# Optimization experiments

Measured on AMD Instinct MI355X. Metric: run time of the kernel, lower is better.

The kernel has to match this reference:

```python
import jax, jax.numpy as jnp
import numpy as np

K_KNN = 20
TC = 3  # taylor_channel
N_TERMS = 20  # trivariate polynomial terms up to order 3
CHANNELS = [(6, 32), (32, 64), (64, 128), (128, 256)]


def _knn_indices(xyz, k):
    sq = jnp.sum(xyz * xyz, axis=1)  # B x N
    d2 = sq[:, :, None] + sq[:, None, :] - 2.0 * jnp.einsum('bci,bcj->bij', xyz, xyz)
    _, idx = jax.lax.top_k(-d2, k)
    return idx


def _group(feat, idx):
    # feat: B x C x N, idx: B x N x K -> B x C x N x K
    return jax.vmap(lambda f, i: f[:, i])(feat, idx)


def _taylor_terms(g):
    X, Y, Z = g[:, 0], g[:, 1], g[:, 2]
    one = jnp.ones_like(X)
    terms = [one, X, Y, Z, X * Y, X * Z, Y * Z, X * X, Y * Y, Z * Z,
             X * X * Y, X * X * Z, X * Y * Y, Y * Y * Z, X * Z * Z, Y * Z * Z,
             X * Y * Z, X * X * X, Y * Y * Y, Z * Z * Z]
    return jnp.stack(terms, axis=1)


def _spider_conv(feat, idx, terms, w1, b1, w2, b2):
    # feat: B x C x N; w1: tc x 20; w2: out x (C*tc) x K
    B, C, N = feat.shape
    g = _group(feat, idx)  # B x C x N x K
    taylor = jnp.einsum('btnk,ot->bonk', terms, w1) + b1[None, :, None, None]
    g = (g[:, :, None, :, :] * taylor[:, None, :, :, :]).reshape(B, C * TC, N, g.shape[-1])
    out = jnp.einsum('bcnk,ock->bon', g, w2) + b2[None, :, None]
    return jax.nn.relu(out)


def _forward(pc, params):
    # pc: B x N x 6
    pcT = jnp.transpose(pc, (0, 2, 1))
    xyz = pcT[:, 0:3, :]
    idx = _knn_indices(xyz, K_KNN)  # B x N x K
    grouped_xyz = _group(xyz, idx)
    grouped_pc = grouped_xyz - xyz[:, :, :, None]  # relative coords
    terms = _taylor_terms(grouped_pc)
    feat = pcT
    feats = []
    for l in range(4):
        w1, b1, w2, b2 = params[l]
        feat = _spider_conv(feat, idx, terms, w1, b1, w2, b2)
        feats.append(feat)
    cat = jnp.concatenate(feats, axis=1)
    top2, _ = jax.lax.top_k(cat, 2)  # topk over point dim (last axis)
    return top2.reshape(cat.shape[0], -1)  # B x 960


def setup_inputs() -> dict:
    key = jax.random.key(0)
    keys = jax.random.split(key, 1 + 16)
    B, N = 4, 2048
    inp = {'pc': jax.random.normal(keys[0], (B, N, 6), dtype=jnp.float32)}
    ki = 1
    for l, (cin, cout) in enumerate(CHANNELS):
        inp[f'w1_{l}'] = jax.random.normal(keys[ki], (TC, N_TERMS), dtype=jnp.float32) * 0.1; ki += 1
        inp[f'b1_{l}'] = jax.random.normal(keys[ki], (TC,), dtype=jnp.float32) * 0.01; ki += 1
        inp[f'w2_{l}'] = jax.random.normal(keys[ki], (cout, cin * TC, K_KNN), dtype=jnp.float32) * (1.0 / np.sqrt(cin * TC * K_KNN)); ki += 1
        inp[f'b2_{l}'] = jax.random.normal(keys[ki], (cout,), dtype=jnp.float32) * 0.01; ki += 1
    return inp


def reference(pc, w1_0, b1_0, w2_0, b2_0, w1_1, b1_1, w2_1, b2_1,
              w1_2, b1_2, w2_2, b2_2, w1_3, b1_3, w2_3, b2_3):
    params = [(w1_0, b1_0, w2_0, b2_0), (w1_1, b1_1, w2_1, b2_1),
              (w1_2, b1_2, w2_2, b2_2), (w1_3, b1_3, w2_3, b2_3)]
    return _forward(pc, params)
```

## Files before the change

### kernel.cpp

```cpp
#include <hip/hip_runtime.h>
#include <math.h>

#define BB 4
#define NN 2048
#define KNN 20

typedef _Float16 f16x8 __attribute__((ext_vector_type(8)));
typedef _Float16 f16x4 __attribute__((ext_vector_type(4)));
typedef _Float16 f16x2 __attribute__((ext_vector_type(2)));
typedef float f32x4 __attribute__((ext_vector_type(4)));

#define DPP_STEP(CTRL, RMASK)                                                   \
    {                                                                           \
        unsigned ov = (unsigned)__builtin_amdgcn_update_dpp(                    \
            (int)bv, (int)bv, CTRL, RMASK, 0xf, false);                         \
        unsigned oj = (unsigned)__builtin_amdgcn_update_dpp(                    \
            (int)jj, (int)jj, CTRL, RMASK, 0xf, false);                         \
        bool lt = (ov < bv) || (ov == bv && oj < jj);                           \
        bv = lt ? ov : bv;                                                      \
        jj = lt ? oj : jj;                                                      \
    }

__global__ __launch_bounds__(256) void knn_kernel(const float* __restrict__ pc,
                                                  int* __restrict__ idx_out,
                                                  float* __restrict__ rel_out) {
    __shared__ float sx[NN], sy[NN], sz[NN], sq[NN];
    const int tid = threadIdx.x;
    const int b = blockIdx.x / (NN / 4);
    const int grp = blockIdx.x % (NN / 4);
    for (int p = tid; p < NN; p += 256) {
        float x = pc[(size_t)(b * NN + p) * 6 + 0];
        float y = pc[(size_t)(b * NN + p) * 6 + 1];
        float z = pc[(size_t)(b * NN + p) * 6 + 2];
        sx[p] = x; sy[p] = y; sz[p] = z;
        sq[p] = __fadd_rn(__fadd_rn(__fmul_rn(x, x), __fmul_rn(y, y)), __fmul_rn(z, z));
    }
    __syncthreads();
    const int lane = tid & 63;
    const int i = grp * 4 + (tid >> 6);
    const float xi = sx[i], yi = sy[i], zi = sz[i];
    const float sqi = sq[i];

    unsigned mmr[32];
#pragma unroll
    for (int t = 0; t < 32; ++t) {
        const int j = t * 64 + lane;
        float dot = __fadd_rn(__fadd_rn(__fmul_rn(xi, sx[j]), __fmul_rn(yi, sy[j])),
                              __fmul_rn(zi, sz[j]));
        float d2 = __fsub_rn(__fadd_rn(sqi, sq[j]), __fmul_rn(2.0f, dot));
        unsigned bbits = __float_as_uint(d2);
        mmr[t] = bbits ^ (0x80000000u | (unsigned)((int)bbits >> 31));
    }

    const unsigned UMAX = 0xFFFFFFFFu;
    unsigned mask = 0u;
    unsigned v1, t1, v2, t2;

    auto refill = [&]() {
        v1 = UMAX; t1 = 0u; v2 = UMAX; t2 = 0u;
#pragma unroll
        for (int t = 0; t < 32; ++t) {
            unsigned m = ((mask >> t) & 1u) ? UMAX : mmr[t];
            bool c1 = m < v1;
            bool c2 = m < v2;
            unsigned nv2 = c1 ? v1 : (c2 ? m : v2);
            unsigned nt2 = c1 ? t1 : (c2 ? (unsigned)t : t2);
            v1 = c1 ? m : v1;
            t1 = c1 ? (unsigned)t : t1;
            v2 = nv2; t2 = nt2;
        }
    };
    refill();

    const size_t orow = (size_t)(b * NN + i);
    for (int k = 0; k < KNN; ++k) {
        unsigned bv = v1;
        unsigned jj = (t1 << 6) | (unsigned)lane;
        DPP_STEP(0x111, 0xf)
        DPP_STEP(0x112, 0xf)
        DPP_STEP(0x114, 0xf)
        DPP_STEP(0x118, 0xf)
        DPP_STEP(0x142, 0xa)
        DPP_STEP(0x143, 0xc)
        const unsigned sj = (unsigned)__builtin_amdgcn_readlane((int)jj, 63);
        if (lane == 0) {
            idx_out[orow * KNN + k] = (int)sj;
            size_t ro = (orow * KNN + k) * 3;
            rel_out[ro + 0] = __fsub_rn(sx[sj], xi);
            rel_out[ro + 1] = __fsub_rn(sy[sj], yi);
            rel_out[ro + 2] = __fsub_rn(sz[sj], zi);
        }
        if (k < KNN - 1) {
            bool am = ((sj & 63u) == (unsigned)lane);
            if (am) {
                mask |= (1u << (sj >> 6));
                v1 = v2; t1 = t2; v2 = UMAX;
            }
            if (__ballot(v1 == UMAX) != 0ull) refill();
        }
    }
}

__global__ __launch_bounds__(256) void taylor_all_kernel(
    const float* __restrict__ rel,
    const float* __restrict__ w10, const float* __restrict__ b10, float* __restrict__ ty0,
    const float* __restrict__ w11, const float* __restrict__ b11, float* __restrict__ ty1,
    const float* __restrict__ w12, const float* __restrict__ b12, float* __restrict__ ty2,
    const float* __restrict__ w13, const float* __restrict__ b13, float* __restrict__ ty3) {
    __shared__ float w1s[4][60];
    __shared__ float b1s[4][3];
    const int tid = threadIdx.x;
    if (tid < 240) {
        const float* wp = (tid < 60) ? w10 : (tid < 120) ? w11 : (tid < 180) ? w12 : w13;
        w1s[tid / 60][tid % 60] = wp[tid % 60];
    } else if (tid < 252) {
        int r = tid - 240;
        const float* bp = (r < 3) ? b10 : (r < 6) ? b11 : (r < 9) ? b12 : b13;
        b1s[r / 3][r % 3] = bp[r % 3];
    }
    __syncthreads();
    int t = blockIdx.x * 256 + tid;
    if (t >= BB * NN * KNN) return;
    float X = rel[(size_t)t * 3 + 0], Y = rel[(size_t)t * 3 + 1], Z = rel[(size_t)t * 3 + 2];
    float tm[20];
    tm[0] = 1.f; tm[1] = X; tm[2] = Y; tm[3] = Z;
    tm[4] = X * Y; tm[5] = X * Z; tm[6] = Y * Z;
    tm[7] = X * X; tm[8] = Y * Y; tm[9] = Z * Z;
    tm[10] = X * X * Y; tm[11] = X * X * Z; tm[12] = X * Y * Y; tm[13] = Y * Y * Z;
    tm[14] = X * Z * Z; tm[15] = Y * Z * Z; tm[16] = X * Y * Z;
    tm[17] = X * X * X; tm[18] = Y * Y * Y; tm[19] = Z * Z * Z;
    float* typ[4] = {ty0, ty1, ty2, ty3};
#pragma unroll
    for (int l = 0; l < 4; ++l) {
#pragma unroll
        for (int o = 0; o < 3; ++o) {
            float a = b1s[l][o];
#pragma unroll
            for (int q = 0; q < 20; ++q) a += w1s[l][o * 20 + q] * tm[q];
            typ[l][(size_t)t * 3 + o] = a;
        }
    }
}

struct WsplitArgs {
    const float* w2[4];
    _Float16* wf[4];
    int COUT[4], CIN[4], CPAD[4], OCB[4], KCB[4];
    int cum[4];
};

__global__ __launch_bounds__(256) void wsplit_all_kernel(WsplitArgs a) {
    int e = blockIdx.x * 256 + threadIdx.x;
    if (e >= a.cum[3]) return;
    int l = (e >= a.cum[0]) + (e >= a.cum[1]) + (e >= a.cum[2]);
    int base = l ? a.cum[l - 1] : 0;
    e -= base;
    const int KCB = a.KCB[l], OCB = a.OCB[l], CPAD = a.CPAD[l], CIN = a.CIN[l];
    int i = e & 7;
    int lane = (e >> 3) & 63;
    int fi = e >> 9;
    int kcb = fi % KCB;
    int ocb = (fi / KCB) % OCB;
    int k = fi / (KCB * OCB);
    int oc = ocb * 16 + (lane & 15);
    int kk = kcb * 32 + (lane >> 4) * 8 + i;
    int o = kk / CPAD, c = kk % CPAD;
    float x = 0.f;
    if (o < 3 && c < CIN)
        x = a.w2[l][((size_t)oc * (CIN * 3) + c * 3 + o) * KNN + k];
    a.wf[l][e] = (_Float16)x;
}

template <int CIN, int COUT, int CK3P, int NT, int WM, int WN, int FM, int FN,
          int OCT, int KSPLIT, bool L0S>
__global__ __launch_bounds__(256) void convm_kernel(const float* __restrict__ fin,
                                                    const int* __restrict__ idx,
                                                    const float* __restrict__ tyg,
                                                    const _Float16* __restrict__ wf,
                                                    float* __restrict__ out) {
    constexpr int KR = KNN / KSPLIT;
    constexpr int SR = CK3P + 8;
    constexpr int KCB = CK3P / 32;
    constexpr int OCB = COUT / 16;
    constexpr int OCBLK = WM * FM * 16;
    constexpr int NTL = NN / NT;
    constexpr int TPR = 256 / NT;
    constexpr int CT = L0S ? 6 : (CIN / TPR);
    constexpr int CQ = L0S ? 2 : (CT / 4);
    static_assert(WN * FN * 16 == NT, "n tiling");
    static_assert(OCBLK * OCT == COUT, "oc tiling");
    static_assert(WM * WN == 4, "4 waves");
    static_assert(OCT * KSPLIT == 4 && NTL == 32 && NT == 64, "xcd decode");

    __shared__ _Float16 Bs[NT * SR];
    __shared__ _Float16 tyt[NT][3 * KR];
    __shared__ int idxt[NT][KR];

    const int tid = threadIdx.x;
    const int lane = tid & 63;
    const int wid = tid >> 6;
    const int wm = wid / WN;
    const int wn = wid % WN;
    const int bid = blockIdx.x;
    const int e_ = (bid & 7) >> 1;
    const int oct = e_ / KSPLIT;
    const int ks = e_ % KSPLIT;
    const int hi = ((bid >> 3) << 1) | (bid & 1);
    const int ntl = hi & 31;
    const int b = hi >> 5;
    const int n0 = ntl * NT;
    const int oc0 = oct * OCBLK;
    const int k0 = ks * KR;
    const size_t brow = (size_t)b * NN;

    for (int e = tid; e < NT * KR; e += 256) {
        int n = e / KR, kk = e % KR;
        idxt[n][kk] = idx[(brow + n0 + n) * KNN + k0 + kk];
    }
    for (int e = tid; e < NT * 3 * KR; e += 256) {
        int n = e / (3 * KR), q = e % (3 * KR);
        tyt[n][q] = (_Float16)tyg[((brow + n0 + n) * KNN + k0) * 3 + q];
    }
    __syncthreads();

    const int nrow = tid & 63;
    const int sub = tid >> 6;
    float4 g[CQ];

    auto issue_gather = [&](int kk) {
        if constexpr (L0S) {
            if (tid < 192) {
                int j = idxt[nrow][kk];
                const float* p = fin + (brow + j) * 6;
                g[0] = *reinterpret_cast<const float4*>(p);
                float2 r2 = *reinterpret_cast<const float2*>(p + 4);
                g[1].x = r2.x; g[1].y = r2.y;
            }
        } else {
            int j = idxt[nrow][kk];
            const float* p = fin + (brow + j) * CIN + sub * CT;
#pragma unroll
            for (int q = 0; q < CQ; ++q)
                g[q] = *reinterpret_cast<const float4*>(p + q * 4);
        }
    };
    issue_gather(0);

    f32x4 acc[FM][FN];
#pragma unroll
    for (int fm = 0; fm < FM; ++fm)
#pragma unroll
        for (int fn = 0; fn < FN; ++fn) acc[fm][fn] = (f32x4){0.f, 0.f, 0.f, 0.f};

    auto loadA = [&](int k, int kcb, f16x8* a) {
#pragma unroll
        for (int fm = 0; fm < FM; ++fm) {
            size_t fidx = ((size_t)k * OCB + (oc0 >> 4) + wm * FM + fm) * KCB + kcb;
            a[fm] = *reinterpret_cast<const f16x8*>(&wf[(fidx * 64 + lane) * 8]);
        }
    };
    auto loadB = [&](int kcb, f16x8* bb) {
#pragma unroll
        for (int fn = 0; fn < FN; ++fn) {
            int row = wn * FN * 16 + fn * 16 + (lane & 15);
            bb[fn] = *reinterpret_cast<const f16x8*>(
                &Bs[row * SR + kcb * 32 + (lane >> 4) * 8]);
        }
    };

    for (int kk = 0; kk < KR; ++kk) {
        const int k = k0 + kk;
        __syncthreads();
        if constexpr (L0S) {
            if (tid < 192) {
                _Float16 th = tyt[nrow][kk * 3 + sub];
                f16x2 tb; tb[0] = th; tb[1] = th;
                f16x2 g0, g1, g2;
                g0[0] = (_Float16)g[0].x; g0[1] = (_Float16)g[0].y;
                g1[0] = (_Float16)g[0].z; g1[1] = (_Float16)g[0].w;
                g2[0] = (_Float16)g[1].x; g2[1] = (_Float16)g[1].y;
                f16x2 p0 = g0 * tb, p1 = g1 * tb, p2 = g2 * tb;
                f16x8 hv;
                hv[0] = p0[0]; hv[1] = p0[1]; hv[2] = p1[0]; hv[3] = p1[1];
                hv[4] = p2[0]; hv[5] = p2[1]; hv[6] = (_Float16)0.f; hv[7] = (_Float16)0.f;
                *reinterpret_cast<f16x8*>(&Bs[nrow * SR + sub * 8]) = hv;
                if (sub == 0) {
                    f16x8 z = {};
                    *reinterpret_cast<f16x8*>(&Bs[nrow * SR + 24]) = z;
                }
            }
        } else {
            f16x2 gh[CT / 2];
#pragma unroll
            for (int q = 0; q < CQ; ++q) {
                f16x2 a0, a1;
                a0[0] = (_Float16)g[q].x; a0[1] = (_Float16)g[q].y;
                a1[0] = (_Float16)g[q].z; a1[1] = (_Float16)g[q].w;
                gh[2 * q] = a0; gh[2 * q + 1] = a1;
            }
            _Float16 th0 = tyt[nrow][kk * 3 + 0];
            _Float16 th1 = tyt[nrow][kk * 3 + 1];
            _Float16 th2 = tyt[nrow][kk * 3 + 2];
#pragma unroll
            for (int o = 0; o < 3; ++o) {
                _Float16 th = (o == 0) ? th0 : (o == 1) ? th1 : th2;
                f16x2 tb; tb[0] = th; tb[1] = th;
#pragma unroll
                for (int qp = 0; qp < CT / 8; ++qp) {
                    f16x2 p0 = gh[4 * qp + 0] * tb;
                    f16x2 p1 = gh[4 * qp + 1] * tb;
                    f16x2 p2 = gh[4 * qp + 2] * tb;
                    f16x2 p3 = gh[4 * qp + 3] * tb;
                    f16x8 hv;
                    hv[0] = p0[0]; hv[1] = p0[1]; hv[2] = p1[0]; hv[3] = p1[1];
                    hv[4] = p2[0]; hv[5] = p2[1]; hv[6] = p3[0]; hv[7] = p3[1];
                    *reinterpret_cast<f16x8*>(
                        &Bs[nrow * SR + o * CIN + sub * CT + qp * 8]) = hv;
                }
            }
        }
        __syncthreads();
        if (kk + 1 < KR) issue_gather(kk + 1);
        f16x8 aC[FM], bC[FN], aN[FM], bN[FN];
        loadA(k, 0, aC);
        loadB(0, bC);
#pragma unroll
        for (int kcb = 0; kcb < KCB; ++kcb) {
            if (kcb + 1 < KCB) { loadA(k, kcb + 1, aN); loadB(kcb + 1, bN); }
#pragma unroll
            for (int fm = 0; fm < FM; ++fm)
#pragma unroll
                for (int fn = 0; fn < FN; ++fn)
                    acc[fm][fn] = __builtin_amdgcn_mfma_f32_16x16x32_f16(
                        aC[fm], bC[fn], acc[fm][fn], 0, 0, 0);
            if (kcb + 1 < KCB) {
#pragma unroll
                for (int fm = 0; fm < FM; ++fm) aC[fm] = aN[fm];
#pragma unroll
                for (int fn = 0; fn < FN; ++fn) bC[fn] = bN[fn];
            }
        }
    }
    float* dst = out + (size_t)ks * ((size_t)BB * NN * COUT);
#pragma unroll
    for (int fm = 0; fm < FM; ++fm) {
        const int ocb = oc0 + wm * FM * 16 + fm * 16 + ((lane >> 4) << 2);
#pragma unroll
        for (int fn = 0; fn < FN; ++fn) {
            int n = n0 + wn * FN * 16 + fn * 16 + (lane & 15);
            float4 o4;
            o4.x = acc[fm][fn][0]; o4.y = acc[fm][fn][1];
            o4.z = acc[fm][fn][2]; o4.w = acc[fm][fn][3];
            *reinterpret_cast<float4*>(&dst[(brow + n) * COUT + ocb]) = o4;
        }
    }
}

template <int COUT, int KS>
__global__ __launch_bounds__(256) void combine_kernel(const float* __restrict__ p,
                                                      const float* __restrict__ b2,
                                                      float* __restrict__ out) {
    constexpr size_t TOT = (size_t)BB * NN * COUT;
    size_t i = (size_t)blockIdx.x * 256 + threadIdx.x;
    if (i * 4 >= TOT) return;
    const float4* p4 = reinterpret_cast<const float4*>(p);
    float4 a = p4[i];
#pragma unroll
    for (int s = 1; s < KS; ++s) {
        float4 v = p4[i + s * (TOT / 4)];
        a.x += v.x; a.y += v.y; a.z += v.z; a.w += v.w;
    }
    float4 bb = *reinterpret_cast<const float4*>(&b2[(i * 4) % COUT]);
    float4 r;
    r.x = fmaxf(a.x + bb.x, 0.f); r.y = fmaxf(a.y + bb.y, 0.f);
    r.z = fmaxf(a.z + bb.z, 0.f); r.w = fmaxf(a.w + bb.w, 0.f);
    reinterpret_cast<float4*>(out)[i] = r;
}

__global__ __launch_bounds__(256) void top2_kernel(const float* __restrict__ f1,
                                                   const float* __restrict__ f2,
                                                   const float* __restrict__ f3,
                                                   const float* __restrict__ p3,
                                                   const float* __restrict__ b23,
                                                   float* __restrict__ out) {
    __shared__ float m1s[256], m2s[256];
    const int bid = blockIdx.x;
    const int b = bid / 480;
    const int ch = bid % 480;
    const size_t brow = (size_t)b * NN;
    float m1 = -INFINITY, m2 = -INFINITY;
    if (ch < 224) {
        const float* f; int C, c;
        if (ch < 32)       { f = f1; C = 32;  c = ch; }
        else if (ch < 96)  { f = f2; C = 64;  c = ch - 32; }
        else               { f = f3; C = 128; c = ch - 96; }
        for (int n = threadIdx.x; n < NN; n += 256) {
            float v = f[(brow + n) * C + c];
            if (v > m1) { m2 = m1; m1 = v; }
            else if (v > m2) m2 = v;
        }
    } else {
        const int c = ch - 224;
        const float bc = b23[c];
        constexpr size_t TOT3 = (size_t)BB * NN * 256;
        for (int n = threadIdx.x; n < NN; n += 256) {
            size_t o = (brow + n) * 256 + c;
            float v = fmaxf(p3[o] + p3[TOT3 + o] + bc, 0.f);
            if (v > m1) { m2 = m1; m1 = v; }
            else if (v > m2) m2 = v;
        }
    }
    m1s[threadIdx.x] = m1; m2s[threadIdx.x] = m2;
    __syncthreads();
    for (int s = 128; s > 0; s >>= 1) {
        if (threadIdx.x < s) {
            float a1 = m1s[threadIdx.x], a2 = m2s[threadIdx.x];
            float c1 = m1s[threadIdx.x + s], c2 = m2s[threadIdx.x + s];
            m1s[threadIdx.x] = fmaxf(a1, c1);
            m2s[threadIdx.x] = fmaxf(fminf(a1, c1), fmaxf(a2, c2));
        }
        __syncthreads();
    }
    if (threadIdx.x == 0) {
        out[(size_t)b * 960 + ch * 2 + 0] = m1s[0];
        out[(size_t)b * 960 + ch * 2 + 1] = m2s[0];
    }
}

extern "C" void kernel_launch(void* const* d_in, const int* in_sizes, int n_in,
                              void* d_out, int out_size, void* d_ws, size_t ws_size,
                              hipStream_t stream) {
    const float* pc = (const float*)d_in[0];
    const float *w1[4], *b1[4], *w2[4], *b2[4];
    for (int l = 0; l < 4; ++l) {
        w1[l] = (const float*)d_in[1 + 4 * l];
        b1[l] = (const float*)d_in[2 + 4 * l];
        w2[l] = (const float*)d_in[3 + 4 * l];
        b2[l] = (const float*)d_in[4 + 4 * l];
    }
    char* ws = (char*)d_ws;
    size_t off = 0;
    auto alloc = [&](size_t bytes) -> void* {
        void* p = ws + off;
        off = (off + bytes + 255) & ~(size_t)255;
        return p;
    };
    int* idxb     = (int*)alloc((size_t)BB * NN * KNN * 4);
    float* rel    = (float*)alloc((size_t)BB * NN * KNN * 3 * 4);
    float* ty0    = (float*)alloc((size_t)BB * NN * KNN * 3 * 4);
    float* ty1    = (float*)alloc((size_t)BB * NN * KNN * 3 * 4);
    float* ty2    = (float*)alloc((size_t)BB * NN * KNN * 3 * 4);
    float* ty3    = (float*)alloc((size_t)BB * NN * KNN * 3 * 4);
    const int wtot0 = KNN * 2 * 1 * 512;
    const int wtot1 = KNN * 4 * 3 * 512;
    const int wtot2 = KNN * 8 * 6 * 512;
    const int wtot3 = KNN * 16 * 12 * 512;
    _Float16* wf0 = (_Float16*)alloc((size_t)wtot0 * 2);
    _Float16* wf1 = (_Float16*)alloc((size_t)wtot1 * 2);
    _Float16* wf2 = (_Float16*)alloc((size_t)wtot2 * 2);
    _Float16* wf3 = (_Float16*)alloc((size_t)wtot3 * 2);
    float* f1     = (float*)alloc((size_t)BB * NN * 32 * 4);
    float* f2     = (float*)alloc((size_t)BB * NN * 64 * 4);
    float* f3     = (float*)alloc((size_t)BB * NN * 128 * 4);
    float* pbuf   = (float*)alloc((size_t)4 * BB * NN * 128 * 4);

    knn_kernel<<<BB * NN / 4, 256, 0, stream>>>(pc, idxb, rel);

    taylor_all_kernel<<<(BB * NN * KNN + 255) / 256, 256, 0, stream>>>(
        rel, w1[0], b1[0], ty0, w1[1], b1[1], ty1, w1[2], b1[2], ty2, w1[3], b1[3], ty3);

    WsplitArgs wa;
    wa.w2[0] = w2[0]; wa.w2[1] = w2[1]; wa.w2[2] = w2[2]; wa.w2[3] = w2[3];
    wa.wf[0] = wf0; wa.wf[1] = wf1; wa.wf[2] = wf2; wa.wf[3] = wf3;
    int COUTs[4] = {32, 64, 128, 256}, CINs[4] = {6, 32, 64, 128};
    int CPADs[4] = {8, 32, 64, 128}, OCBs[4] = {2, 4, 8, 16}, KCBs[4] = {1, 3, 6, 12};
    int cum = 0;
    for (int l = 0; l < 4; ++l) {
        wa.COUT[l] = COUTs[l]; wa.CIN[l] = CINs[l]; wa.CPAD[l] = CPADs[l];
        wa.OCB[l] = OCBs[l]; wa.KCB[l] = KCBs[l];
        cum += KNN * OCBs[l] * KCBs[l] * 512;
        wa.cum[l] = cum;
    }
    wsplit_all_kernel<<<(cum + 255) / 256, 256, 0, stream>>>(wa);

    convm_kernel<6, 32, 32, 64, 2, 2, 1, 2, 1, 4, true>
        <<<512, 256, 0, stream>>>(pc, idxb, ty0, wf0, pbuf);
    combine_kernel<32, 4><<<(BB * NN * 32 / 4 + 255) / 256, 256, 0, stream>>>(pbuf, b2[0], f1);

    convm_kernel<32, 64, 96, 64, 4, 1, 1, 4, 1, 4, false>
        <<<512, 256, 0, stream>>>(f1, idxb, ty1, wf1, pbuf);
    combine_kernel<64, 4><<<(BB * NN * 64 / 4 + 255) / 256, 256, 0, stream>>>(pbuf, b2[1], f2);

    convm_kernel<64, 128, 192, 64, 4, 1, 2, 4, 1, 4, false>
        <<<512, 256, 0, stream>>>(f2, idxb, ty2, wf2, pbuf);
    combine_kernel<128, 4><<<(BB * NN * 128 / 4 + 255) / 256, 256, 0, stream>>>(pbuf, b2[2], f3);

    convm_kernel<128, 256, 384, 64, 4, 1, 2, 4, 2, 2, false>
        <<<512, 256, 0, stream>>>(f3, idxb, ty3, wf3, pbuf);

    top2_kernel<<<BB * 480, 256, 0, stream>>>(f1, f2, f3, pbuf, b2[3], (float*)d_out);
}
```

Measured before the change: 202.2 us.

## Add per-taylor-channel conv kernel for layers 2-3 and store taylor terms in fp16

Adds a convo_kernel for the two largest layers. It builds the B tile in shared memory one Taylor output channel at a time, so the tile is CIN wide instead of 3*CIN. Each layer now uses 1024 blocks with a smaller oc tile and launch_bounds occupancy 4. Taylor coefficients are written as fp16, halving that traffic, and block index decoding switches from the XCD-aware mapping to plain div/mod. The trade-off is more __syncthreads per neighbour step and the loss of the XCD-locality swizzle.

```diff
diff --git a/kernel.cpp b/kernel.cpp
--- a/kernel.cpp
+++ b/kernel.cpp
@@ -103,10 +103,10 @@
 
 __global__ __launch_bounds__(256) void taylor_all_kernel(
     const float* __restrict__ rel,
-    const float* __restrict__ w10, const float* __restrict__ b10, float* __restrict__ ty0,
-    const float* __restrict__ w11, const float* __restrict__ b11, float* __restrict__ ty1,
-    const float* __restrict__ w12, const float* __restrict__ b12, float* __restrict__ ty2,
-    const float* __restrict__ w13, const float* __restrict__ b13, float* __restrict__ ty3) {
+    const float* __restrict__ w10, const float* __restrict__ b10, _Float16* __restrict__ ty0,
+    const float* __restrict__ w11, const float* __restrict__ b11, _Float16* __restrict__ ty1,
+    const float* __restrict__ w12, const float* __restrict__ b12, _Float16* __restrict__ ty2,
+    const float* __restrict__ w13, const float* __restrict__ b13, _Float16* __restrict__ ty3) {
     __shared__ float w1s[4][60];
     __shared__ float b1s[4][3];
     const int tid = threadIdx.x;
@@ -129,7 +129,7 @@
     tm[10] = X * X * Y; tm[11] = X * X * Z; tm[12] = X * Y * Y; tm[13] = Y * Y * Z;
     tm[14] = X * Z * Z; tm[15] = Y * Z * Z; tm[16] = X * Y * Z;
     tm[17] = X * X * X; tm[18] = Y * Y * Y; tm[19] = Z * Z * Z;
-    float* typ[4] = {ty0, ty1, ty2, ty3};
+    _Float16* typ[4] = {ty0, ty1, ty2, ty3};
 #pragma unroll
     for (int l = 0; l < 4; ++l) {
 #pragma unroll
@@ -137,7 +137,7 @@
             float a = b1s[l][o];
 #pragma unroll
             for (int q = 0; q < 20; ++q) a += w1s[l][o * 20 + q] * tm[q];
-            typ[l][(size_t)t * 3 + o] = a;
+            typ[l][(size_t)t * 3 + o] = (_Float16)a;
         }
     }
 }
@@ -175,7 +175,7 @@
           int OCT, int KSPLIT, bool L0S>
 __global__ __launch_bounds__(256) void convm_kernel(const float* __restrict__ fin,
                                                     const int* __restrict__ idx,
-                                                    const float* __restrict__ tyg,
+                                                    const _Float16* __restrict__ tyg,
                                                     const _Float16* __restrict__ wf,
                                                     float* __restrict__ out) {
     constexpr int KR = KNN / KSPLIT;
@@ -190,7 +190,6 @@
     static_assert(WN * FN * 16 == NT, "n tiling");
     static_assert(OCBLK * OCT == COUT, "oc tiling");
     static_assert(WM * WN == 4, "4 waves");
-    static_assert(OCT * KSPLIT == 4 && NTL == 32 && NT == 64, "xcd decode");
 
     __shared__ _Float16 Bs[NT * SR];
     __shared__ _Float16 tyt[NT][3 * KR];
@@ -201,13 +200,11 @@
     const int wid = tid >> 6;
     const int wm = wid / WN;
     const int wn = wid % WN;
-    const int bid = blockIdx.x;
-    const int e_ = (bid & 7) >> 1;
-    const int oct = e_ / KSPLIT;
-    const int ks = e_ % KSPLIT;
-    const int hi = ((bid >> 3) << 1) | (bid & 1);
-    const int ntl = hi & 31;
-    const int b = hi >> 5;
+    int t = blockIdx.x;
+    const int ks = t % KSPLIT; t /= KSPLIT;
+    const int oct = t % OCT;   t /= OCT;
+    const int ntl = t % NTL;   t /= NTL;
+    const int b = t;
     const int n0 = ntl * NT;
     const int oc0 = oct * OCBLK;
     const int k0 = ks * KR;
@@ -219,7 +216,7 @@
     }
     for (int e = tid; e < NT * 3 * KR; e += 256) {
         int n = e / (3 * KR), q = e % (3 * KR);
-        tyt[n][q] = (_Float16)tyg[((brow + n0 + n) * KNN + k0) * 3 + q];
+        tyt[n][q] = tyg[((brow + n0 + n) * KNN + k0) * 3 + q];
     }
     __syncthreads();
 
@@ -338,6 +335,152 @@
                 for (int fm = 0; fm < FM; ++fm) aC[fm] = aN[fm];
 #pragma unroll
                 for (int fn = 0; fn < FN; ++fn) bC[fn] = bN[fn];
+            }
+        }
+    }
+    float* dst = out + (size_t)ks * ((size_t)BB * NN * COUT);
+#pragma unroll
+    for (int fm = 0; fm < FM; ++fm) {
+        const int ocb = oc0 + wm * FM * 16 + fm * 16 + ((lane >> 4) << 2);
+#pragma unroll
+        for (int fn = 0; fn < FN; ++fn) {
+            int n = n0 + wn * FN * 16 + fn * 16 + (lane & 15);
+            float4 o4;
+            o4.x = acc[fm][fn][0]; o4.y = acc[fm][fn][1];
+            o4.z = acc[fm][fn][2]; o4.w = acc[fm][fn][3];
+            *reinterpret_cast<float4*>(&dst[(brow + n) * COUT + ocb]) = o4;
+        }
+    }
+}
+
+template <int CIN, int COUT, int OCBLK, int KSPLIT, int WM, int WN, int FM, int FN>
+__global__ __launch_bounds__(256, 4) void convo_kernel(const float* __restrict__ fin,
+                                                       const int* __restrict__ idx,
+                                                       const _Float16* __restrict__ tyg,
+                                                       const _Float16* __restrict__ wf,
+                                                       float* __restrict__ out) {
+    constexpr int KR = KNN / KSPLIT;
+    constexpr int OCT = COUT / OCBLK;
+    constexpr int NT = 64;
+    constexpr int TPR = 4;
+    constexpr int CT = CIN / TPR;
+    constexpr int CQ = CT / 4;
+    constexpr int SRo = CIN + 8;
+    constexpr int KCBo = CIN / 32;
+    constexpr int KCB = 3 * KCBo;
+    constexpr int OCB = COUT / 16;
+    static_assert(WM * FM * 16 == OCBLK, "oc tiling");
+    static_assert(WN * FN * 16 == NT, "n tiling");
+    static_assert(WM * WN == 4, "4 waves");
+
+    __shared__ _Float16 Bs[NT * SRo];
+    __shared__ _Float16 tyt[NT][3 * KR];
+    __shared__ int idxt[NT][KR];
+
+    const int tid = threadIdx.x;
+    const int lane = tid & 63;
+    const int wid = tid >> 6;
+    const int wm = wid / WN;
+    const int wn = wid % WN;
+    int t = blockIdx.x;
+    const int ks = t % KSPLIT; t /= KSPLIT;
+    const int oct = t % OCT;   t /= OCT;
+    const int ntl = t % 32;    t /= 32;
+    const int b = t;
+    const int n0 = ntl * NT;
+    const int oc0 = oct * OCBLK;
+    const int k0 = ks * KR;
+    const size_t brow = (size_t)b * NN;
+
+    for (int e = tid; e < NT * KR; e += 256) {
+        int n = e / KR, kk = e % KR;
+        idxt[n][kk] = idx[(brow + n0 + n) * KNN + k0 + kk];
+    }
+    for (int e = tid; e < NT * 3 * KR; e += 256) {
+        int n = e / (3 * KR), q = e % (3 * KR);
+        tyt[n][q] = tyg[((brow + n0 + n) * KNN + k0) * 3 + q];
+    }
+    __syncthreads();
+
+    const int nrow = tid & 63;
+    const int sub = tid >> 6;
+    float4 g[CQ];
+
+    auto issue_gather = [&](int kk) {
+        int j = idxt[nrow][kk];
+        const float* p = fin + (brow + j) * CIN + sub * CT;
+#pragma unroll
+        for (int q = 0; q < CQ; ++q)
+            g[q] = *reinterpret_cast<const float4*>(p + q * 4);
+    };
+    issue_gather(0);
+
+    f32x4 acc[FM][FN];
+#pragma unroll
+    for (int fm = 0; fm < FM; ++fm)
+#pragma unroll
+        for (int fn = 0; fn < FN; ++fn) acc[fm][fn] = (f32x4){0.f, 0.f, 0.f, 0.f};
+
+    f16x8 areg[FM * KCBo];
+    auto loadA = [&](int k, int o) {
+#pragma unroll
+        for (int fm = 0; fm < FM; ++fm)
+#pragma unroll
+            for (int kcb = 0; kcb < KCBo; ++kcb) {
+                size_t fidx = ((size_t)k * OCB + (oc0 >> 4) + wm * FM + fm) * KCB +
+                              o * KCBo + kcb;
+                areg[fm * KCBo + kcb] =
+                    *reinterpret_cast<const f16x8*>(&wf[(fidx * 64 + lane) * 8]);
+            }
+    };
+
+    for (int kk = 0; kk < KR; ++kk) {
+        const int k = k0 + kk;
+        f16x2 gh[CT / 2];
+#pragma unroll
+        for (int q = 0; q < CQ; ++q) {
+            f16x2 a0, a1;
+            a0[0] = (_Float16)g[q].x; a0[1] = (_Float16)g[q].y;
+            a1[0] = (_Float16)g[q].z; a1[1] = (_Float16)g[q].w;
+            gh[2 * q] = a0; gh[2 * q + 1] = a1;
+        }
+        if (kk + 1 < KR) issue_gather(kk + 1);
+        _Float16 th0 = tyt[nrow][kk * 3 + 0];
+        _Float16 th1 = tyt[nrow][kk * 3 + 1];
+        _Float16 th2 = tyt[nrow][kk * 3 + 2];
+#pragma unroll 1
+        for (int o = 0; o < 3; ++o) {
+            loadA(k, o);
+            __syncthreads();
+            _Float16 th = (o == 0) ? th0 : (o == 1) ? th1 : th2;
+            f16x2 tb; tb[0] = th; tb[1] = th;
+#pragma unroll
+            for (int qp = 0; qp < CT / 8; ++qp) {
+                f16x2 p0 = gh[4 * qp + 0] * tb;
+                f16x2 p1 = gh[4 * qp + 1] * tb;
+                f16x2 p2 = gh[4 * qp + 2] * tb;
+                f16x2 p3 = gh[4 * qp + 3] * tb;
+                f16x8 hv;
+                hv[0] = p0[0]; hv[1] = p0[1]; hv[2] = p1[0]; hv[3] = p1[1];
+                hv[4] = p2[0]; hv[5] = p2[1]; hv[6] = p3[0]; hv[7] = p3[1];
+                *reinterpret_cast<f16x8*>(&Bs[nrow * SRo + sub * CT + qp * 8]) = hv;
+            }
+            __syncthreads();
+#pragma unroll
+            for (int kcb = 0; kcb < KCBo; ++kcb) {
+                f16x8 bf[FN];
+#pragma unroll
+                for (int fn = 0; fn < FN; ++fn) {
+                    int row = wn * FN * 16 + fn * 16 + (lane & 15);
+                    bf[fn] = *reinterpret_cast<const f16x8*>(
+                        &Bs[row * SRo + kcb * 32 + (lane >> 4) * 8]);
+                }
+#pragma unroll
+                for (int fm = 0; fm < FM; ++fm)
+#pragma unroll
+                    for (int fn = 0; fn < FN; ++fn)
+                        acc[fm][fn] = __builtin_amdgcn_mfma_f32_16x16x32_f16(
+                            areg[fm * KCBo + kcb], bf[fn], acc[fm][fn], 0, 0, 0);
             }
         }
     }
@@ -445,12 +588,12 @@
         off = (off + bytes + 255) & ~(size_t)255;
         return p;
     };
-    int* idxb     = (int*)alloc((size_t)BB * NN * KNN * 4);
-    float* rel    = (float*)alloc((size_t)BB * NN * KNN * 3 * 4);
-    float* ty0    = (float*)alloc((size_t)BB * NN * KNN * 3 * 4);
-    float* ty1    = (float*)alloc((size_t)BB * NN * KNN * 3 * 4);
-    float* ty2    = (float*)alloc((size_t)BB * NN * KNN * 3 * 4);
-    float* ty3    = (float*)alloc((size_t)BB * NN * KNN * 3 * 4);
+    int* idxb      = (int*)alloc((size_t)BB * NN * KNN * 4);
+    float* rel     = (float*)alloc((size_t)BB * NN * KNN * 3 * 4);
+    _Float16* ty0  = (_Float16*)alloc((size_t)BB * NN * KNN * 3 * 2);
+    _Float16* ty1  = (_Float16*)alloc((size_t)BB * NN * KNN * 3 * 2);
+    _Float16* ty2  = (_Float16*)alloc((size_t)BB * NN * KNN * 3 * 2);
+    _Float16* ty3  = (_Float16*)alloc((size_t)BB * NN * KNN * 3 * 2);
     const int wtot0 = KNN * 2 * 1 * 512;
     const int wtot1 = KNN * 4 * 3 * 512;
     const int wtot2 = KNN * 8 * 6 * 512;
@@ -491,12 +634,12 @@
         <<<512, 256, 0, stream>>>(f1, idxb, ty1, wf1, pbuf);
     combine_kernel<64, 4><<<(BB * NN * 64 / 4 + 255) / 256, 256, 0, stream>>>(pbuf, b2[1], f2);
 
-    convm_kernel<64, 128, 192, 64, 4, 1, 2, 4, 1, 4, false>
-        <<<512, 256, 0, stream>>>(f2, idxb, ty2, wf2, pbuf);
+    convo_kernel<64, 128, 64, 4, 2, 2, 2, 2>
+        <<<1024, 256, 0, stream>>>(f2, idxb, ty2, wf2, pbuf);
     combine_kernel<128, 4><<<(BB * NN * 128 / 4 + 255) / 256, 256, 0, stream>>>(pbuf, b2[2], f3);
 
-    convm_kernel<128, 256, 384, 64, 4, 1, 2, 4, 2, 2, false>
-        <<<512, 256, 0, stream>>>(f3, idxb, ty3, wf3, pbuf);
+    convo_kernel<128, 256, 64, 2, 2, 2, 2, 2>
+        <<<1024, 256, 0, stream>>>(f3, idxb, ty3, wf3, pbuf);
 
     top2_kernel<<<BB * 480, 256, 0, stream>>>(f1, f2, f3, pbuf, b2[3], (float*)d_out);
 }
```

After: 225.3 us. 11.4% more time.
